# Kernel tuning notes

Hardware: AMD Instinct MI355X
Metric: run time of the kernel (lower is better)

Reference implementation:

```python
import jax, jax.numpy as jnp
import numpy as np

NUM_EXPERTS = 3
INPUT_DIM = 1024
HIDDEN_DIM = 4096
OUTPUT_DIM = 1024
ROUTER_HIDDEN = 128
BATCH = 8192


def setup_inputs() -> dict:
    key = jax.random.key(0)
    ks = jax.random.split(key, 6)
    s_in = 1.0 / np.sqrt(INPUT_DIM)
    s_h = 1.0 / np.sqrt(HIDDEN_DIM)
    s_rh = 1.0 / np.sqrt(ROUTER_HIDDEN)
    return {
        "x": jax.random.normal(ks[0], (BATCH, INPUT_DIM), jnp.float32),
        "router_w1": jax.random.normal(ks[1], (INPUT_DIM, ROUTER_HIDDEN), jnp.float32) * s_in,
        "router_b1": jnp.zeros((ROUTER_HIDDEN,), jnp.float32),
        "router_w2": jax.random.normal(ks[2], (ROUTER_HIDDEN, NUM_EXPERTS), jnp.float32) * s_rh,
        "router_b2": jnp.zeros((NUM_EXPERTS,), jnp.float32),
        "expert_w1": jax.random.normal(ks[3], (NUM_EXPERTS, INPUT_DIM, HIDDEN_DIM), jnp.float32) * s_in,
        "expert_b1": jnp.zeros((NUM_EXPERTS, HIDDEN_DIM), jnp.float32),
        "expert_w2": jax.random.normal(ks[4], (NUM_EXPERTS, HIDDEN_DIM, OUTPUT_DIM), jnp.float32) * s_h,
        "expert_b2": jnp.zeros((NUM_EXPERTS, OUTPUT_DIM), jnp.float32),
    }


def reference(x, router_w1, router_b1, router_w2, router_b2,
              expert_w1, expert_b1, expert_w2, expert_b2):
    # Router: MLP -> softmax probs, hard top-1 selection (argmax)
    rh = jax.nn.relu(x @ router_w1 + router_b1)          # [B, 128]
    logits = rh @ router_w2 + router_b2                   # [B, E]
    probs = jax.nn.softmax(logits, axis=-1)
    selected = jnp.argmax(probs, axis=-1)                 # [B] int

    # Per-expert forward on all tokens (dense equivalent of masked dispatch)
    h = jax.nn.relu(jnp.einsum('bi,eih->ebh', x, expert_w1) + expert_b1[:, None, :])  # [E,B,H]
    y = jnp.einsum('ebh,eho->ebo', h, expert_w2) + expert_b2[:, None, :]              # [E,B,O]

    # Scatter-combine: each token takes its selected expert's output
    outputs = jnp.take_along_axis(
        y, selected[None, :, None], axis=0)[0]            # [B, O]

    # routing_stats: tokens per expert
    routing_stats = jnp.bincount(selected, length=NUM_EXPERTS)
    return outputs, routing_stats
```

## Files before the change

kernel.cpp:

```cpp
#include <hip/hip_runtime.h>
#include <hip/hip_bf16.h>

typedef short bf16x8 __attribute__((ext_vector_type(8)));
typedef float f32x4 __attribute__((ext_vector_type(4)));
typedef __attribute__((address_space(1))) const void gconst_t;
typedef __attribute__((address_space(3))) void lds_t;

#define DEVI __device__ __forceinline__

constexpr int BATCH   = 8192;
constexpr int IN_DIM  = 1024;
constexpr int HID     = 4096;
constexpr int OUT_DIM = 1024;
constexpr int NE      = 3;

constexpr size_t XBF_OFF  = 0;
constexpr size_t W1T_OFF  = 16777216;
constexpr size_t W2T_OFF  = W1T_OFF + 25165824;
constexpr size_t H_OFF    = W2T_OFF + 25165824;
constexpr size_t META_OFF = H_OFF + 67108864;

DEVI unsigned short f2bf(float f) {
  __hip_bfloat16 h = __float2bfloat16(f);
  return *reinterpret_cast<unsigned short*>(&h);
}

__global__ __launch_bounds__(256) void router_kernel(
    const float* __restrict__ x, const float* __restrict__ rw1, const float* __restrict__ rb1,
    const float* __restrict__ rw2, const float* __restrict__ rb2,
    int* __restrict__ counts, int* __restrict__ toklist) {
  __shared__ float wbuf[2][64 * 128];
  __shared__ float xbuf[2][16 * 64];
  const int tid = threadIdx.x;
  const int t0 = blockIdx.x * 16;
  const int hcol = tid & 127;
  const int g = tid >> 7;

  const float* wsrc = rw1 + (size_t)tid * 4;
  const float* xsrc = x + (size_t)(t0 + (tid >> 4)) * 1024 + (tid & 15) * 4;
  const unsigned soff = (unsigned)tid * 16u;

  auto STAGE = [&](int buf, int c) {
#pragma unroll
    for (int j = 0; j < 8; j++)
      __builtin_amdgcn_global_load_lds((gconst_t*)(wsrc + (size_t)c * 8192 + j * 1024),
                                       (lds_t*)((char*)&wbuf[buf][0] + j * 4096 + soff), 16, 0, 0);
    __builtin_amdgcn_global_load_lds((gconst_t*)(xsrc + c * 64),
                                     (lds_t*)((char*)&xbuf[buf][0] + soff), 16, 0, 0);
  };

  float acc[8] = {0.f, 0.f, 0.f, 0.f, 0.f, 0.f, 0.f, 0.f};

  STAGE(0, 0);
  for (int c = 0; c < 16; ++c) {
    asm volatile("s_waitcnt vmcnt(0)" ::: "memory");
    __builtin_amdgcn_sched_barrier(0);
    __builtin_amdgcn_s_barrier();
    __builtin_amdgcn_sched_barrier(0);
    if (c + 1 < 16) STAGE((c + 1) & 1, c + 1);
    const float* wb = &wbuf[c & 1][0];
    const float* xb = &xbuf[c & 1][0];
    for (int kk = 0; kk < 64; kk += 4) {
      const float w0 = wb[(kk + 0) * 128 + hcol];
      const float w1v = wb[(kk + 1) * 128 + hcol];
      const float w2v = wb[(kk + 2) * 128 + hcol];
      const float w3v = wb[(kk + 3) * 128 + hcol];
#pragma unroll
      for (int tt = 0; tt < 8; tt++) {
        const float4 xv = *(const float4*)&xb[(g * 8 + tt) * 64 + kk];
        acc[tt] = fmaf(xv.x, w0, acc[tt]);
        acc[tt] = fmaf(xv.y, w1v, acc[tt]);
        acc[tt] = fmaf(xv.z, w2v, acc[tt]);
        acc[tt] = fmaf(xv.w, w3v, acc[tt]);
      }
    }
  }

  __syncthreads();
  float* rh = &wbuf[0][0];
  const float bb1 = rb1[hcol];
#pragma unroll
  for (int tt = 0; tt < 8; tt++)
    rh[(g * 8 + tt) * 132 + hcol] = fmaxf(acc[tt] + bb1, 0.f);
  __syncthreads();
  float* lg = &xbuf[0][0];
  if (tid < 48) {
    const int t = tid / 3, e = tid % 3;
    float s = rb2[e];
    for (int j = 0; j < 128; j++) s = fmaf(rh[t * 132 + j], rw2[j * 3 + e], s);
    lg[t * 3 + e] = s;
  }
  __syncthreads();
  if (tid < 16) {
    const float l0 = lg[tid * 3], l1 = lg[tid * 3 + 1], l2 = lg[tid * 3 + 2];
    int sel = 0; float m = l0;
    if (l1 > m) { m = l1; sel = 1; }
    if (l2 > m) { m = l2; sel = 2; }
    const int slot = atomicAdd(&counts[sel], 1);
    toklist[sel * BATCH + slot] = t0 + tid;
  }
}

__global__ __launch_bounds__(256) void prep2_kernel(
    const float* __restrict__ x, const float* __restrict__ ew1, const float* __restrict__ ew2,
    unsigned short* __restrict__ xb, unsigned short* __restrict__ w1t,
    unsigned short* __restrict__ w2t) {
  __shared__ float tile[64][65];
  const int b = blockIdx.x;
  const int tid = threadIdx.x;

  if (b < 6144) {
    const float* src; unsigned short* dst; int R, C, r0, c0;
    if (b < 3072) {
      const int e = b / 1024, w = b % 1024;
      src = ew1 + (size_t)e * 1024 * 4096; dst = w1t + (size_t)e * 4096 * 1024;
      R = 1024; C = 4096; r0 = (w & 15) * 64; c0 = (w >> 4) * 64;
    } else {
      const int bb = b - 3072, e = bb / 1024, w = bb % 1024;
      src = ew2 + (size_t)e * 4096 * 1024; dst = w2t + (size_t)e * 1024 * 4096;
      R = 4096; C = 1024; r0 = (w & 63) * 64; c0 = (w >> 6) * 64;
    }
    const int tr = tid >> 4;
    const int tc = (tid & 15) << 2;
#pragma unroll
    for (int i = 0; i < 4; i++) {
      const int r = tr + i * 16;
      const float4 v = *(const float4*)(src + (size_t)(r0 + r) * C + (c0 + tc));
      tile[r][tc + 0] = v.x; tile[r][tc + 1] = v.y; tile[r][tc + 2] = v.z; tile[r][tc + 3] = v.w;
    }
    __syncthreads();
#pragma unroll
    for (int i = 0; i < 4; i++) {
      const int c = tr + i * 16;
      ushort4 o;
      o.x = f2bf(tile[tc + 0][c]);
      o.y = f2bf(tile[tc + 1][c]);
      o.z = f2bf(tile[tc + 2][c]);
      o.w = f2bf(tile[tc + 3][c]);
      *(ushort4*)(dst + (size_t)(c0 + c) * R + (r0 + tc)) = o;
    }
  } else {
    const float4* xv4 = (const float4*)x;
    const int total = BATCH * IN_DIM / 4;
    for (int i = (b - 6144) * 256 + tid; i < total; i += 512 * 256) {
      const float4 v = xv4[i];
      ushort4 o;
      o.x = f2bf(v.x); o.y = f2bf(v.y); o.z = f2bf(v.z); o.w = f2bf(v.w);
      ((ushort4*)xb)[i] = o;
    }
  }
}

template <int MODE>
__global__ __launch_bounds__(512, 2) void moe_gemm(
    const unsigned short* __restrict__ Abase, const unsigned short* __restrict__ Ball,
    const float* __restrict__ biasAll, unsigned short* __restrict__ Hout,
    float* __restrict__ Yout, const int* __restrict__ toklist, const int* __restrict__ counts,
    float* __restrict__ tail) {
  constexpr int N  = (MODE == 0) ? HID : OUT_DIM;
  constexpr int K  = (MODE == 0) ? IN_DIM : HID;
  constexpr int NT = K / 32;

  const int tid = threadIdx.x;
  if (MODE == 0 && blockIdx.x == 0 && blockIdx.y == 0 && tid < NE)
    tail[tid] = (float)counts[tid];

  const int c0 = counts[0], c1 = counts[1], c2 = counts[2];
  const int mb0 = (c0 + 127) >> 7, mb1 = (c1 + 127) >> 7, mb2 = (c2 + 127) >> 7;
  const int bx = blockIdx.x;
  int e, mblk;
  if (bx < mb0) { e = 0; mblk = bx; }
  else if (bx < mb0 + mb1) { e = 1; mblk = bx - mb0; }
  else if (bx < mb0 + mb1 + mb2) { e = 2; mblk = bx - mb0 - mb1; }
  else return;
  const int cnt = (e == 0) ? c0 : (e == 1) ? c1 : c2;
  const int m0 = mblk * 128;
  const int n0 = blockIdx.y * 256;
  const int off_e = (e > 0 ? c0 : 0) + (e > 1 ? c1 : 0);
  const unsigned short* Bmat = Ball + (size_t)e * ((size_t)N * K);
  const float* bias = biasAll + (size_t)e * N;

  __shared__ unsigned short Ab[3][128 * 32];
  __shared__ unsigned short Bb[3][256 * 32];

  const unsigned short* asrc;
  const unsigned short* bsrc[2];
  unsigned aoff, boff[2];
  {
    const unsigned o = (unsigned)tid * 16u;
    const unsigned p = o ^ (((o >> 6) & 3u) << 4);
    const int row = (int)(o >> 6);
    const int kel = (int)((p & 63u) >> 1);
    aoff = o;
    int slot = m0 + row; if (slot > cnt - 1) slot = cnt - 1;
    const size_t arow = (MODE == 0) ? (size_t)toklist[e * BATCH + slot]
                                    : (size_t)(off_e + slot);
    asrc = Abase + arow * K + kel;
  }
#pragma unroll
  for (int l = 0; l < 2; l++) {
    const unsigned o = l * 8192u + (unsigned)tid * 16u;
    const unsigned p = o ^ (((o >> 6) & 3u) << 4);
    const int row = (int)(o >> 6);
    const int kel = (int)((p & 63u) >> 1);
    boff[l] = o;
    bsrc[l] = Bmat + (size_t)(n0 + row) * K + kel;
  }

  f32x4 acc[4][4];
#pragma unroll
  for (int i = 0; i < 4; i++)
#pragma unroll
    for (int j = 0; j < 4; j++) acc[i][j] = {0.f, 0.f, 0.f, 0.f};

  const int lane = tid & 63;
  const int wave = tid >> 6;
  const int wm = (wave >> 2) * 64;
  const int wn = (wave & 3) * 64;
  const int fr = lane & 15;
  const int fc = lane >> 4;

  auto STAGE = [&](int buf, int kofs) {
    __builtin_amdgcn_global_load_lds((gconst_t*)(asrc + kofs),
                                     (lds_t*)((char*)&Ab[buf][0] + aoff), 16, 0, 0);
#pragma unroll
    for (int l = 0; l < 2; l++)
      __builtin_amdgcn_global_load_lds((gconst_t*)(bsrc[l] + kofs),
                                       (lds_t*)((char*)&Bb[buf][0] + boff[l]), 16, 0, 0);
  };

  STAGE(0, 0);
  STAGE(1, 32);

  int cur = 0;
  for (int t = 0; t < NT; ++t) {
    if (t + 1 < NT) asm volatile("s_waitcnt vmcnt(3)" ::: "memory");
    else            asm volatile("s_waitcnt vmcnt(0)" ::: "memory");
    __builtin_amdgcn_sched_barrier(0);
    __builtin_amdgcn_s_barrier();
    __builtin_amdgcn_sched_barrier(0);
    bf16x8 af[4], bv[4];
#pragma unroll
    for (int m = 0; m < 4; m++) {
      const unsigned row = (unsigned)(wm + m * 16 + fr);
      const unsigned addr = ((row << 6) + (unsigned)(fc << 4)) ^ ((row & 3u) << 4);
      af[m] = *(const bf16x8*)((const char*)&Ab[cur][0] + addr);
    }
#pragma unroll
    for (int n = 0; n < 4; n++) {
      const unsigned row = (unsigned)(wn + n * 16 + fr);
      const unsigned addr = ((row << 6) + (unsigned)(fc << 4)) ^ ((row & 3u) << 4);
      bv[n] = *(const bf16x8*)((const char*)&Bb[cur][0] + addr);
    }
    asm volatile("s_waitcnt lgkmcnt(0)" ::: "memory");
    __builtin_amdgcn_sched_barrier(0);
    __builtin_amdgcn_s_setprio(1);
#pragma unroll
    for (int m = 0; m < 4; m++)
#pragma unroll
      for (int n = 0; n < 4; n++)
        acc[m][n] = __builtin_amdgcn_mfma_f32_16x16x32_bf16(af[m], bv[n], acc[m][n], 0, 0, 0);
    __builtin_amdgcn_s_setprio(0);
    if (t + 2 < NT) {
      const int nb = (cur + 2 >= 3) ? cur - 1 : cur + 2;
      STAGE(nb, (t + 2) * 32);
    }
    cur = (cur + 1 == 3) ? 0 : cur + 1;
  }

  const int crow = (lane >> 4) * 4;
  const int ccol = lane & 15;
#pragma unroll
  for (int mi = 0; mi < 4; mi++) {
#pragma unroll
    for (int r = 0; r < 4; r++) {
      const int slot = m0 + wm + mi * 16 + crow + r;
      if (slot >= cnt) continue;
      if (MODE == 0) {
        unsigned short* hrow = Hout + (size_t)(off_e + slot) * HID;
#pragma unroll
        for (int ni = 0; ni < 4; ni++) {
          const int n = n0 + wn + ni * 16 + ccol;
          const float v = acc[mi][ni][r] + bias[n];
          hrow[n] = f2bf(fmaxf(v, 0.f));
        }
      } else {
        const int tok = toklist[e * BATCH + slot];
        float* yrow = Yout + (size_t)tok * OUT_DIM;
#pragma unroll
        for (int ni = 0; ni < 4; ni++) {
          const int n = n0 + wn + ni * 16 + ccol;
          yrow[n] = acc[mi][ni][r] + bias[n];
        }
      }
    }
  }
}

extern "C" void kernel_launch(void* const* d_in, const int* in_sizes, int n_in,
                              void* d_out, int out_size, void* d_ws, size_t ws_size,
                              hipStream_t stream) {
  const float* x   = (const float*)d_in[0];
  const float* rw1 = (const float*)d_in[1];
  const float* rb1 = (const float*)d_in[2];
  const float* rw2 = (const float*)d_in[3];
  const float* rb2 = (const float*)d_in[4];
  const float* ew1 = (const float*)d_in[5];
  const float* eb1 = (const float*)d_in[6];
  const float* ew2 = (const float*)d_in[7];
  const float* eb2 = (const float*)d_in[8];
  float* out = (float*)d_out;

  char* ws = (char*)d_ws;
  unsigned short* xb  = (unsigned short*)(ws + XBF_OFF);
  unsigned short* w1t = (unsigned short*)(ws + W1T_OFF);
  unsigned short* w2t = (unsigned short*)(ws + W2T_OFF);
  unsigned short* h   = (unsigned short*)(ws + H_OFF);
  int* counts  = (int*)(ws + META_OFF);
  int* toklist = counts + 16;
  float* tail = out + (size_t)BATCH * OUT_DIM;

  hipMemsetAsync(counts, 0, 64, stream);
  router_kernel<<<512, 256, 0, stream>>>(x, rw1, rb1, rw2, rb2, counts, toklist);
  prep2_kernel<<<6656, 256, 0, stream>>>(x, ew1, ew2, xb, w1t, w2t);
  moe_gemm<0><<<dim3(66, 16), 512, 0, stream>>>(xb, w1t, eb1, h, nullptr, toklist, counts, tail);
  moe_gemm<1><<<dim3(66, 4), 512, 0, stream>>>(h, w2t, eb2, nullptr, out, toklist, counts, tail);
}
```

Baseline: 394.4 us.

## Compute router layer on MFMA using split bf16 hi/lo emulation of fp32

Replaces the scalar FP32 router GEMM with an MFMA bf16 kernel that approximates fp32 accuracy using a three-term hi/lo split (xhi*whi + xlo*whi + xhi*wlo), concatenated along K into a 3072-long reduction. A new prep kernel converts x to bf16 hi and lo parts and transposes rw1 into a packed [128,3072] hi/hi/lo layout. The x bf16 conversion moves out of prep2 into this prep kernel. The router now runs 128 tokens per block over 64 blocks with a three-buffer global-to-LDS pipeline. The aim is to cut router cost, at the risk of argmax flips from reduced precision and fewer blocks in flight.

```diff
diff --git a/kernel.cpp b/kernel.cpp
--- a/kernel.cpp
+++ b/kernel.cpp
@@ -18,136 +18,253 @@
 constexpr size_t W1T_OFF  = 16777216;
 constexpr size_t W2T_OFF  = W1T_OFF + 25165824;
 constexpr size_t H_OFF    = W2T_OFF + 25165824;
+constexpr size_t XLO_OFF  = H_OFF;
 constexpr size_t META_OFF = H_OFF + 67108864;
+constexpr size_t W3_OFF   = META_OFF + 131072;
 
 DEVI unsigned short f2bf(float f) {
   __hip_bfloat16 h = __float2bfloat16(f);
   return *reinterpret_cast<unsigned short*>(&h);
 }
-
-__global__ __launch_bounds__(256) void router_kernel(
-    const float* __restrict__ x, const float* __restrict__ rw1, const float* __restrict__ rb1,
+DEVI float bf2f(unsigned short u) {
+  unsigned v = (unsigned)u << 16;
+  return __uint_as_float(v);
+}
+
+__global__ __launch_bounds__(256) void prepA_kernel(
+    const float* __restrict__ x, const float* __restrict__ rw1,
+    unsigned short* __restrict__ xb, unsigned short* __restrict__ xlo,
+    unsigned short* __restrict__ w3) {
+  __shared__ float tile[64][65];
+  const int b = blockIdx.x;
+  const int tid = threadIdx.x;
+  if (b < 512) {
+    const float4* xv4 = (const float4*)x;
+    const int total = BATCH * IN_DIM / 4;
+    for (int i = b * 256 + tid; i < total; i += 512 * 256) {
+      const float4 v = xv4[i];
+      ushort4 h, l;
+      h.x = f2bf(v.x); l.x = f2bf(v.x - bf2f(h.x));
+      h.y = f2bf(v.y); l.y = f2bf(v.y - bf2f(h.y));
+      h.z = f2bf(v.z); l.z = f2bf(v.z - bf2f(h.z));
+      h.w = f2bf(v.w); l.w = f2bf(v.w - bf2f(h.w));
+      ((ushort4*)xb)[i] = h;
+      ((ushort4*)xlo)[i] = l;
+    }
+  } else {
+    const int w = b - 512;
+    const int r0 = (w >> 1) * 64;
+    const int c0 = (w & 1) * 64;
+    const int tr = tid >> 4;
+    const int tc = (tid & 15) << 2;
+#pragma unroll
+    for (int i = 0; i < 4; i++) {
+      const int r = tr + i * 16;
+      const float4 v = *(const float4*)(rw1 + (size_t)(r0 + r) * 128 + (c0 + tc));
+      tile[r][tc + 0] = v.x; tile[r][tc + 1] = v.y; tile[r][tc + 2] = v.z; tile[r][tc + 3] = v.w;
+    }
+    __syncthreads();
+#pragma unroll
+    for (int i = 0; i < 4; i++) {
+      const int c = tr + i * 16;
+      ushort4 hi, lo;
+      {
+        float f;
+        f = tile[tc + 0][c]; hi.x = f2bf(f); lo.x = f2bf(f - bf2f(hi.x));
+        f = tile[tc + 1][c]; hi.y = f2bf(f); lo.y = f2bf(f - bf2f(hi.y));
+        f = tile[tc + 2][c]; hi.z = f2bf(f); lo.z = f2bf(f - bf2f(hi.z));
+        f = tile[tc + 3][c]; hi.w = f2bf(f); lo.w = f2bf(f - bf2f(hi.w));
+      }
+      unsigned short* base = w3 + (size_t)(c0 + c) * 3072 + (r0 + tc);
+      *(ushort4*)(base)        = hi;
+      *(ushort4*)(base + 1024) = hi;
+      *(ushort4*)(base + 2048) = lo;
+    }
+  }
+}
+
+__global__ __launch_bounds__(256) void router_gemm(
+    const unsigned short* __restrict__ xhi, const unsigned short* __restrict__ xlo,
+    const unsigned short* __restrict__ w3, const float* __restrict__ rb1,
     const float* __restrict__ rw2, const float* __restrict__ rb2,
     int* __restrict__ counts, int* __restrict__ toklist) {
-  __shared__ float wbuf[2][64 * 128];
-  __shared__ float xbuf[2][16 * 64];
+  __shared__ __align__(16) char smem[70656];
+  unsigned short* Ab = (unsigned short*)smem;
+  unsigned short* Bb = (unsigned short*)(smem + 24576);
+  float* rhp  = (float*)smem;
+  float* lgp  = (float*)(smem + 67584);
+  float* rw2l = (float*)(smem + 69120);
+
   const int tid = threadIdx.x;
-  const int t0 = blockIdx.x * 16;
-  const int hcol = tid & 127;
-  const int g = tid >> 7;
-
-  const float* wsrc = rw1 + (size_t)tid * 4;
-  const float* xsrc = x + (size_t)(t0 + (tid >> 4)) * 1024 + (tid & 15) * 4;
-  const unsigned soff = (unsigned)tid * 16u;
-
-  auto STAGE = [&](int buf, int c) {
-#pragma unroll
-    for (int j = 0; j < 8; j++)
-      __builtin_amdgcn_global_load_lds((gconst_t*)(wsrc + (size_t)c * 8192 + j * 1024),
-                                       (lds_t*)((char*)&wbuf[buf][0] + j * 4096 + soff), 16, 0, 0);
-    __builtin_amdgcn_global_load_lds((gconst_t*)(xsrc + c * 64),
-                                     (lds_t*)((char*)&xbuf[buf][0] + soff), 16, 0, 0);
+  const int m0 = blockIdx.x * 128;
+  constexpr int NT = 96;
+
+  int tokA[2], kelA[2];
+  unsigned aoff[2];
+  const unsigned short* bsrc[2];
+  unsigned boff[2];
+#pragma unroll
+  for (int l = 0; l < 2; l++) {
+    const unsigned o = l * 4096u + (unsigned)tid * 16u;
+    const unsigned p = o ^ (((o >> 6) & 3u) << 4);
+    const int row = (int)(o >> 6);
+    const int kel = (int)((p & 63u) >> 1);
+    aoff[l] = o;
+    tokA[l] = m0 + row;
+    kelA[l] = kel;
+    boff[l] = o;
+    bsrc[l] = w3 + (size_t)row * 3072 + kel;
+  }
+
+  auto STAGE = [&](int buf, int t) {
+    const int seg = t >> 5;
+    const int kin = (t & 31) * 32;
+    const unsigned short* abase = (seg == 1) ? xlo : xhi;
+#pragma unroll
+    for (int l = 0; l < 2; l++)
+      __builtin_amdgcn_global_load_lds(
+          (gconst_t*)(abase + (size_t)tokA[l] * 1024 + kin + kelA[l]),
+          (lds_t*)((char*)Ab + buf * 8192 + aoff[l]), 16, 0, 0);
+#pragma unroll
+    for (int l = 0; l < 2; l++)
+      __builtin_amdgcn_global_load_lds(
+          (gconst_t*)(bsrc[l] + t * 32),
+          (lds_t*)((char*)Bb + buf * 8192 + boff[l]), 16, 0, 0);
   };
 
-  float acc[8] = {0.f, 0.f, 0.f, 0.f, 0.f, 0.f, 0.f, 0.f};
+  f32x4 acc[4][4];
+#pragma unroll
+  for (int i = 0; i < 4; i++)
+#pragma unroll
+    for (int j = 0; j < 4; j++) acc[i][j] = {0.f, 0.f, 0.f, 0.f};
+
+  const int lane = tid & 63;
+  const int wave = tid >> 6;
+  const int wm = (wave >> 1) * 64;
+  const int wn = (wave & 1) * 64;
+  const int fr = lane & 15;
+  const int fc = lane >> 4;
 
   STAGE(0, 0);
-  for (int c = 0; c < 16; ++c) {
-    asm volatile("s_waitcnt vmcnt(0)" ::: "memory");
+  STAGE(1, 1);
+
+  int cur = 0;
+  for (int t = 0; t < NT; ++t) {
+    if (t + 1 < NT) asm volatile("s_waitcnt vmcnt(4)" ::: "memory");
+    else            asm volatile("s_waitcnt vmcnt(0)" ::: "memory");
     __builtin_amdgcn_sched_barrier(0);
     __builtin_amdgcn_s_barrier();
     __builtin_amdgcn_sched_barrier(0);
-    if (c + 1 < 16) STAGE((c + 1) & 1, c + 1);
-    const float* wb = &wbuf[c & 1][0];
-    const float* xb = &xbuf[c & 1][0];
-    for (int kk = 0; kk < 64; kk += 4) {
-      const float w0 = wb[(kk + 0) * 128 + hcol];
-      const float w1v = wb[(kk + 1) * 128 + hcol];
-      const float w2v = wb[(kk + 2) * 128 + hcol];
-      const float w3v = wb[(kk + 3) * 128 + hcol];
-#pragma unroll
-      for (int tt = 0; tt < 8; tt++) {
-        const float4 xv = *(const float4*)&xb[(g * 8 + tt) * 64 + kk];
-        acc[tt] = fmaf(xv.x, w0, acc[tt]);
-        acc[tt] = fmaf(xv.y, w1v, acc[tt]);
-        acc[tt] = fmaf(xv.z, w2v, acc[tt]);
-        acc[tt] = fmaf(xv.w, w3v, acc[tt]);
+    bf16x8 af[4], bv[4];
+#pragma unroll
+    for (int m = 0; m < 4; m++) {
+      const unsigned row = (unsigned)(wm + m * 16 + fr);
+      const unsigned addr = ((row << 6) + (unsigned)(fc << 4)) ^ ((row & 3u) << 4);
+      af[m] = *(const bf16x8*)((const char*)Ab + cur * 8192 + addr);
+    }
+#pragma unroll
+    for (int n = 0; n < 4; n++) {
+      const unsigned row = (unsigned)(wn + n * 16 + fr);
+      const unsigned addr = ((row << 6) + (unsigned)(fc << 4)) ^ ((row & 3u) << 4);
+      bv[n] = *(const bf16x8*)((const char*)Bb + cur * 8192 + addr);
+    }
+    asm volatile("s_waitcnt lgkmcnt(0)" ::: "memory");
+    __builtin_amdgcn_sched_barrier(0);
+    __builtin_amdgcn_s_setprio(1);
+#pragma unroll
+    for (int m = 0; m < 4; m++)
+#pragma unroll
+      for (int n = 0; n < 4; n++)
+        acc[m][n] = __builtin_amdgcn_mfma_f32_16x16x32_bf16(af[m], bv[n], acc[m][n], 0, 0, 0);
+    __builtin_amdgcn_s_setprio(0);
+    if (t + 2 < NT) {
+      const int nb = (cur + 2 >= 3) ? cur - 1 : cur + 2;
+      STAGE(nb, t + 2);
+    }
+    cur = (cur + 1 == 3) ? 0 : cur + 1;
+  }
+
+  __syncthreads();
+
+  for (int i = tid; i < 384; i += 256) rw2l[i] = rw2[i];
+
+  const int crow = (lane >> 4) * 4;
+  const int ccol = lane & 15;
+  float b1v[4];
+#pragma unroll
+  for (int ni = 0; ni < 4; ni++) b1v[ni] = rb1[wn + ni * 16 + ccol];
+#pragma unroll
+  for (int mi = 0; mi < 4; mi++) {
+#pragma unroll
+    for (int r = 0; r < 4; r++) {
+      const int tokL = wm + mi * 16 + crow + r;
+#pragma unroll
+      for (int ni = 0; ni < 4; ni++) {
+        const int h = wn + ni * 16 + ccol;
+        rhp[tokL * 132 + h] = fmaxf(acc[mi][ni][r] + b1v[ni], 0.f);
       }
     }
   }
-
   __syncthreads();
-  float* rh = &wbuf[0][0];
-  const float bb1 = rb1[hcol];
-#pragma unroll
-  for (int tt = 0; tt < 8; tt++)
-    rh[(g * 8 + tt) * 132 + hcol] = fmaxf(acc[tt] + bb1, 0.f);
+
+#pragma unroll
+  for (int pass = 0; pass < 2; ++pass) {
+    const int t = tid + pass * 256;
+    if (t < 384) {
+      const int tok = t / 3, e = t - tok * 3;
+      float s = rb2[e];
+#pragma unroll 4
+      for (int j = 0; j < 128; ++j) s = fmaf(rhp[tok * 132 + j], rw2l[j * 3 + e], s);
+      lgp[tok * 3 + e] = s;
+    }
+  }
   __syncthreads();
-  float* lg = &xbuf[0][0];
-  if (tid < 48) {
-    const int t = tid / 3, e = tid % 3;
-    float s = rb2[e];
-    for (int j = 0; j < 128; j++) s = fmaf(rh[t * 132 + j], rw2[j * 3 + e], s);
-    lg[t * 3 + e] = s;
-  }
-  __syncthreads();
-  if (tid < 16) {
-    const float l0 = lg[tid * 3], l1 = lg[tid * 3 + 1], l2 = lg[tid * 3 + 2];
+
+  if (tid < 128) {
+    const float l0 = lgp[tid * 3], l1 = lgp[tid * 3 + 1], l2 = lgp[tid * 3 + 2];
     int sel = 0; float m = l0;
     if (l1 > m) { m = l1; sel = 1; }
     if (l2 > m) { m = l2; sel = 2; }
     const int slot = atomicAdd(&counts[sel], 1);
-    toklist[sel * BATCH + slot] = t0 + tid;
+    toklist[sel * BATCH + slot] = m0 + tid;
   }
 }
 
 __global__ __launch_bounds__(256) void prep2_kernel(
-    const float* __restrict__ x, const float* __restrict__ ew1, const float* __restrict__ ew2,
-    unsigned short* __restrict__ xb, unsigned short* __restrict__ w1t,
-    unsigned short* __restrict__ w2t) {
+    const float* __restrict__ ew1, const float* __restrict__ ew2,
+    unsigned short* __restrict__ w1t, unsigned short* __restrict__ w2t) {
   __shared__ float tile[64][65];
   const int b = blockIdx.x;
   const int tid = threadIdx.x;
 
-  if (b < 6144) {
-    const float* src; unsigned short* dst; int R, C, r0, c0;
-    if (b < 3072) {
-      const int e = b / 1024, w = b % 1024;
-      src = ew1 + (size_t)e * 1024 * 4096; dst = w1t + (size_t)e * 4096 * 1024;
-      R = 1024; C = 4096; r0 = (w & 15) * 64; c0 = (w >> 4) * 64;
-    } else {
-      const int bb = b - 3072, e = bb / 1024, w = bb % 1024;
-      src = ew2 + (size_t)e * 4096 * 1024; dst = w2t + (size_t)e * 1024 * 4096;
-      R = 4096; C = 1024; r0 = (w & 63) * 64; c0 = (w >> 6) * 64;
-    }
-    const int tr = tid >> 4;
-    const int tc = (tid & 15) << 2;
-#pragma unroll
-    for (int i = 0; i < 4; i++) {
-      const int r = tr + i * 16;
-      const float4 v = *(const float4*)(src + (size_t)(r0 + r) * C + (c0 + tc));
-      tile[r][tc + 0] = v.x; tile[r][tc + 1] = v.y; tile[r][tc + 2] = v.z; tile[r][tc + 3] = v.w;
-    }
-    __syncthreads();
-#pragma unroll
-    for (int i = 0; i < 4; i++) {
-      const int c = tr + i * 16;
-      ushort4 o;
-      o.x = f2bf(tile[tc + 0][c]);
-      o.y = f2bf(tile[tc + 1][c]);
-      o.z = f2bf(tile[tc + 2][c]);
-      o.w = f2bf(tile[tc + 3][c]);
-      *(ushort4*)(dst + (size_t)(c0 + c) * R + (r0 + tc)) = o;
-    }
+  const float* src; unsigned short* dst; int R, C, r0, c0;
+  if (b < 3072) {
+    const int e = b / 1024, w = b % 1024;
+    src = ew1 + (size_t)e * 1024 * 4096; dst = w1t + (size_t)e * 4096 * 1024;
+    R = 1024; C = 4096; r0 = (w & 15) * 64; c0 = (w >> 4) * 64;
   } else {
-    const float4* xv4 = (const float4*)x;
-    const int total = BATCH * IN_DIM / 4;
-    for (int i = (b - 6144) * 256 + tid; i < total; i += 512 * 256) {
-      const float4 v = xv4[i];
-      ushort4 o;
-      o.x = f2bf(v.x); o.y = f2bf(v.y); o.z = f2bf(v.z); o.w = f2bf(v.w);
-      ((ushort4*)xb)[i] = o;
-    }
+    const int bb = b - 3072, e = bb / 1024, w = bb % 1024;
+    src = ew2 + (size_t)e * 4096 * 1024; dst = w2t + (size_t)e * 1024 * 4096;
+    R = 4096; C = 1024; r0 = (w & 63) * 64; c0 = (w >> 6) * 64;
+  }
+  const int tr = tid >> 4;
+  const int tc = (tid & 15) << 2;
+#pragma unroll
+  for (int i = 0; i < 4; i++) {
+    const int r = tr + i * 16;
+    const float4 v = *(const float4*)(src + (size_t)(r0 + r) * C + (c0 + tc));
+    tile[r][tc + 0] = v.x; tile[r][tc + 1] = v.y; tile[r][tc + 2] = v.z; tile[r][tc + 3] = v.w;
+  }
+  __syncthreads();
+#pragma unroll
+  for (int i = 0; i < 4; i++) {
+    const int c = tr + i * 16;
+    ushort4 o;
+    o.x = f2bf(tile[tc + 0][c]);
+    o.y = f2bf(tile[tc + 1][c]);
+    o.z = f2bf(tile[tc + 2][c]);
+    o.w = f2bf(tile[tc + 3][c]);
+    *(ushort4*)(dst + (size_t)(c0 + c) * R + (r0 + tc)) = o;
   }
 }
 
@@ -316,13 +433,16 @@
   unsigned short* w1t = (unsigned short*)(ws + W1T_OFF);
   unsigned short* w2t = (unsigned short*)(ws + W2T_OFF);
   unsigned short* h   = (unsigned short*)(ws + H_OFF);
+  unsigned short* xlo = (unsigned short*)(ws + XLO_OFF);
   int* counts  = (int*)(ws + META_OFF);
   int* toklist = counts + 16;
+  unsigned short* w3 = (unsigned short*)(ws + W3_OFF);
   float* tail = out + (size_t)BATCH * OUT_DIM;
 
   hipMemsetAsync(counts, 0, 64, stream);
-  router_kernel<<<512, 256, 0, stream>>>(x, rw1, rb1, rw2, rb2, counts, toklist);
-  prep2_kernel<<<6656, 256, 0, stream>>>(x, ew1, ew2, xb, w1t, w2t);
+  prepA_kernel<<<544, 256, 0, stream>>>(x, rw1, xb, xlo, w3);
+  router_gemm<<<64, 256, 0, stream>>>(xb, xlo, w3, rb1, rw2, rb2, counts, toklist);
+  prep2_kernel<<<6144, 256, 0, stream>>>(ew1, ew2, w1t, w2t);
   moe_gemm<0><<<dim3(66, 16), 512, 0, stream>>>(xb, w1t, eb1, h, nullptr, toklist, counts, tail);
   moe_gemm<1><<<dim3(66, 4), 512, 0, stream>>>(h, w2t, eb2, nullptr, out, toklist, counts, tail);
 }
```

Result: faster. 367.7 us (-6.8%).
